# Optimization experiments

Measured on AMD Instinct MI355X. Metric: run time of the kernel, lower is better.

The kernel has to match this reference:

```python
import jax, jax.numpy as jnp
import numpy as np

G, NG, K, D = 64, 2048, 16, 256  # graphs, nodes/graph, eigvecs/graph, feature dim


def setup_inputs() -> dict:
    key = jax.random.key(0)
    k0, k1, k2, k3, k4 = jax.random.split(key, 5)
    x = jax.random.normal(k0, (G * NG, D), jnp.float32)
    # eigenvectors of per-graph Laplacians (values arbitrary for correctness baseline)
    eigvec = jax.random.normal(k1, (G * NG, K), jnp.float32) / np.float32(np.sqrt(NG))
    split_real = jnp.ones((D,), jnp.float32)
    split_imag = jnp.ones((D,), jnp.float32)
    spec_filter = jax.random.uniform(k2, (G, K, D), dtype=jnp.float32)
    W1 = jax.random.normal(k3, (D, D), jnp.float32) / np.float32(np.sqrt(D))
    W2 = jax.random.normal(k4, (D, D), jnp.float32) / np.float32(np.sqrt(D))
    factor_split = jnp.ones((D, 2), jnp.float32)
    return dict(x=x, eigvec=eigvec, split_real=split_real, split_imag=split_imag,
                spec_filter=spec_filter, W1=W1, W2=W2, factor_split=factor_split)


def _silu_norm(h):
    # SiLU gating: sigmoid of complex L2-norm over the spectral (k) axis, keepdim
    norm = jnp.sqrt(jnp.sum(h.real ** 2 + h.imag ** 2, axis=1, keepdims=True))
    return h * jax.nn.sigmoid(norm)


def reference(x, eigvec, split_real, split_imag, spec_filter, W1, W2, factor_split):
    # SpecFeatureTransformLayer (split variant): x -> complex
    xc = jax.lax.complex(split_real * x, split_imag * x)      # [N, D] complex64
    V = eigvec.reshape(G, NG, K)                              # block-diagonal eigvec basis
    xg = xc.reshape(G, NG, D)
    # eigvec^H @ x  (block-diag COO matmul, eigvecs real so conj is a no-op)
    x_spec = jnp.einsum('gnk,gnd->gkd', V, xg)                # [G, K, D] complex64
    x_spec = spec_filter * x_spec                             # learned spectral filter
    # silu_stack: MaybeComplexLinear (same real weight on real & imag) + norm-gated SiLU
    for W in (W1, W2):                                        # W: [out, in], y = x @ W^T
        h = jnp.einsum('gkd,ed->gke', x_spec, W)
        x_spec = _silu_norm(h)
    # project back to node domain: eigvec @ x_spec
    xn = jnp.einsum('gnk,gkd->gnd', V, x_spec).reshape(G * NG, D)
    # real/imag merge via factor_split
    out = xn.real * factor_split[:, 0] + xn.imag * factor_split[:, 1]
    return out + x                                            # node residual
```

## Files before the change

kernel.cpp:

```cpp
#include <hip/hip_runtime.h>
#include <math.h>

#define G  64
#define NG 2048
#define K  16
#define D  256
#define KD (K*D)
#define ROWS 32
#define NCHUNK (NG/ROWS)
#define WPF ((size_t)G * NCHUNK * KD)

typedef float v4f __attribute__((ext_vector_type(4)));

__global__ __launch_bounds__(64) void k_project(const float* __restrict__ x,
                                                const float* __restrict__ eig,
                                                float* __restrict__ WP) {
    __shared__ float sV[ROWS * K];
    const int b  = blockIdx.x;
    const int g  = b >> 6, c = b & 63;
    const int n0 = g * NG + c * ROWS;
    const int t  = threadIdx.x;

    {
        const float4* e4 = (const float4*)(eig + (size_t)n0 * K);
        float4* s4 = (float4*)sV;
        s4[t]      = e4[t];
        s4[t + 64] = e4[t + 64];
    }
    __syncthreads();

    float acc[K][4];
#pragma unroll
    for (int k = 0; k < K; ++k)
#pragma unroll
        for (int j = 0; j < 4; ++j) acc[k][j] = 0.f;

    const float4* x4 = (const float4*)x + (size_t)n0 * 64;
#pragma unroll 4
    for (int n = 0; n < ROWS; ++n) {
        const float4 xv = x4[n * 64 + t];
#pragma unroll
        for (int kq = 0; kq < 4; ++kq) {
            const float4 v = *(const float4*)&sV[n * K + kq * 4];
            acc[kq*4+0][0] += v.x * xv.x; acc[kq*4+0][1] += v.x * xv.y;
            acc[kq*4+0][2] += v.x * xv.z; acc[kq*4+0][3] += v.x * xv.w;
            acc[kq*4+1][0] += v.y * xv.x; acc[kq*4+1][1] += v.y * xv.y;
            acc[kq*4+1][2] += v.y * xv.z; acc[kq*4+1][3] += v.y * xv.w;
            acc[kq*4+2][0] += v.z * xv.x; acc[kq*4+2][1] += v.z * xv.y;
            acc[kq*4+2][2] += v.z * xv.z; acc[kq*4+2][3] += v.z * xv.w;
            acc[kq*4+3][0] += v.w * xv.x; acc[kq*4+3][1] += v.w * xv.y;
            acc[kq*4+3][2] += v.w * xv.z; acc[kq*4+3][3] += v.w * xv.w;
        }
    }

    float4* wp4 = (float4*)WP + (size_t)b * (KD / 4);
#pragma unroll
    for (int k = 0; k < K; ++k)
        wp4[k * 64 + t] = make_float4(acc[k][0], acc[k][1], acc[k][2], acc[k][3]);
}

__global__ __launch_bounds__(256) void k_reduce(const float* __restrict__ WP,
                                                const float* __restrict__ filt,
                                                const float* __restrict__ sr,
                                                const float* __restrict__ si,
                                                float* __restrict__ Xr,
                                                float* __restrict__ Xi) {
    const int b = blockIdx.x;
    const int g = b >> 2, q = b & 3;
    const int f = q * 256 + threadIdx.x;
    const float4* wp4 = (const float4*)WP + (size_t)g * NCHUNK * (KD / 4);
    float ax = 0.f, ay = 0.f, az = 0.f, aw = 0.f;
#pragma unroll 8
    for (int w = 0; w < NCHUNK; ++w) {
        const float4 p = wp4[(size_t)w * (KD / 4) + f];
        ax += p.x; ay += p.y; az += p.z; aw += p.w;
    }
    const float4 fl = ((const float4*)filt)[(size_t)g * (KD / 4) + f];
    const int d4 = f & 63;
    const float4 s0 = ((const float4*)sr)[d4];
    const float4 s1 = ((const float4*)si)[d4];
    float4 xr, xi;
    xr.x = ax * fl.x * s0.x; xr.y = ay * fl.y * s0.y;
    xr.z = az * fl.z * s0.z; xr.w = aw * fl.w * s0.w;
    xi.x = ax * fl.x * s1.x; xi.y = ay * fl.y * s1.y;
    xi.z = az * fl.z * s1.z; xi.w = aw * fl.w * s1.w;
    ((float4*)Xr)[(size_t)g * (KD / 4) + f] = xr;
    ((float4*)Xi)[(size_t)g * (KD / 4) + f] = xi;
}

template <int LAYER>
__global__ __launch_bounds__(256) void k_mlp(const float* __restrict__ Xr,
                                             const float* __restrict__ Xi,
                                             const float* __restrict__ W,
                                             const float* __restrict__ fs,
                                             float* __restrict__ o0,
                                             float* __restrict__ o1) {
    __shared__ float4 sW[64 * 64];
    __shared__ float  sRed[4 * 64 * 8];
    const int b     = blockIdx.x;
    const int g     = b >> 2;
    const int slice = b & 3;
    const int t     = threadIdx.x;

    {
        const float4* Wg = (const float4*)W + (size_t)slice * 64 * 64;
#pragma unroll
        for (int it = 0; it < 16; ++it) {
            const int idx = it * 256 + t;
            const int e = idx >> 6, ds = idx & 63;
            sW[e * 64 + (ds ^ (e & 7))] = Wg[idx];
        }
    }
    __syncthreads();

    const int el = t & 63;
    const int kq = t >> 6;
    const float* xr = Xr + (size_t)g * KD + (kq * 4) * D;
    const float* xi = Xi + (size_t)g * KD + (kq * 4) * D;

    float pr[4] = {0.f, 0.f, 0.f, 0.f};
    float pi[4] = {0.f, 0.f, 0.f, 0.f};
#pragma unroll 4
    for (int ds = 0; ds < 64; ++ds) {
        const float4 w = sW[el * 64 + (ds ^ (el & 7))];
#pragma unroll
        for (int kk = 0; kk < 4; ++kk) {
            const float4 a = *(const float4*)&xr[kk * D + ds * 4];
            const float4 c = *(const float4*)&xi[kk * D + ds * 4];
            pr[kk] += w.x * a.x + w.y * a.y + w.z * a.z + w.w * a.w;
            pi[kk] += w.x * c.x + w.y * c.y + w.z * c.z + w.w * c.w;
        }
    }

#pragma unroll
    for (int kk = 0; kk < 4; ++kk) {
        sRed[(kq * 64 + el) * 8 + kk]     = pr[kk];
        sRed[(kq * 64 + el) * 8 + 4 + kk] = pi[kk];
    }
    __syncthreads();

    if (t < 64) {
        float hr[K], hi[K];
        float nrm = 0.f;
#pragma unroll
        for (int q2 = 0; q2 < 4; ++q2)
#pragma unroll
            for (int kk = 0; kk < 4; ++kk) {
                const float r  = sRed[(q2 * 64 + t) * 8 + kk];
                const float im = sRed[(q2 * 64 + t) * 8 + 4 + kk];
                hr[q2 * 4 + kk] = r; hi[q2 * 4 + kk] = im;
                nrm += r * r + im * im;
            }
        const float sg = 1.f / (1.f + expf(-sqrtf(nrm)));
        const int e = slice * 64 + t;
        if (LAYER == 1) {
#pragma unroll
            for (int k = 0; k < K; ++k) {
                o0[(size_t)g * KD + k * D + e] = hr[k] * sg;
                o1[(size_t)g * KD + k * D + e] = hi[k] * sg;
            }
        } else {
            const float f0 = fs[e * 2], f1 = fs[e * 2 + 1];
#pragma unroll
            for (int k = 0; k < K; ++k)
                o0[(size_t)g * KD + k * D + e] = (hr[k] * sg) * f0 + (hi[k] * sg) * f1;
        }
    }
}

__global__ __launch_bounds__(64) void k_back(const float* __restrict__ x,
                                             const float* __restrict__ eig,
                                             const float* __restrict__ z,
                                             float* __restrict__ out) {
    __shared__ float sV[ROWS * K];
    const int b  = blockIdx.x;
    const int g  = b >> 6, c = b & 63;
    const int n0 = g * NG + c * ROWS;
    const int t  = threadIdx.x;
    {
        const float4* e4 = (const float4*)(eig + (size_t)n0 * K);
        float4* s4 = (float4*)sV;
        s4[t]      = e4[t];
        s4[t + 64] = e4[t + 64];
    }
    float4 zr[K];
    const float4* z4 = (const float4*)z + (size_t)g * (KD / 4);
#pragma unroll
    for (int k = 0; k < K; ++k) zr[k] = z4[k * 64 + t];
    __syncthreads();

    const float4* x4 = (const float4*)x + (size_t)n0 * 64;
    v4f* o4 = (v4f*)out + (size_t)n0 * 64;
#pragma unroll 4
    for (int n = 0; n < ROWS; ++n) {
        float4 o = x4[n * 64 + t];
#pragma unroll
        for (int kq = 0; kq < 4; ++kq) {
            const float4 v = *(const float4*)&sV[n * K + kq * 4];
            o.x += v.x * zr[kq*4+0].x + v.y * zr[kq*4+1].x + v.z * zr[kq*4+2].x + v.w * zr[kq*4+3].x;
            o.y += v.x * zr[kq*4+0].y + v.y * zr[kq*4+1].y + v.z * zr[kq*4+2].y + v.w * zr[kq*4+3].y;
            o.z += v.x * zr[kq*4+0].z + v.y * zr[kq*4+1].z + v.z * zr[kq*4+2].z + v.w * zr[kq*4+3].z;
            o.w += v.x * zr[kq*4+0].w + v.y * zr[kq*4+1].w + v.z * zr[kq*4+2].w + v.w * zr[kq*4+3].w;
        }
        v4f ov; ov.x = o.x; ov.y = o.y; ov.z = o.z; ov.w = o.w;
        __builtin_nontemporal_store(ov, &o4[n * 64 + t]);
    }
}

extern "C" void kernel_launch(void* const* d_in, const int* in_sizes, int n_in,
                              void* d_out, int out_size, void* d_ws, size_t ws_size,
                              hipStream_t stream) {
    const float* x    = (const float*)d_in[0];
    const float* eig  = (const float*)d_in[1];
    const float* sr   = (const float*)d_in[2];
    const float* si   = (const float*)d_in[3];
    const float* filt = (const float*)d_in[4];
    const float* W1   = (const float*)d_in[5];
    const float* W2   = (const float*)d_in[6];
    const float* fs   = (const float*)d_in[7];
    float* out = (float*)d_out;

    float* WP  = out;
    float* Xr  = out + WPF;
    float* Xi  = Xr + (size_t)G * KD;
    float* y1r = Xi + (size_t)G * KD;
    float* y1i = y1r + (size_t)G * KD;
    float* z   = (float*)d_ws;

    k_project<<<G * NCHUNK, 64, 0, stream>>>(x, eig, WP);
    k_reduce<<<G * 4, 256, 0, stream>>>(WP, filt, sr, si, Xr, Xi);
    k_mlp<1><<<G * 4, 256, 0, stream>>>(Xr, Xi, W1, nullptr, y1r, y1i);
    k_mlp<2><<<G * 4, 256, 0, stream>>>(y1r, y1i, W2, fs, z, nullptr);
    k_back<<<G * NCHUNK, 64, 0, stream>>>(x, eig, z, out);
}
```

Measured before the change: 339.0 us.

## Reduce partial sums in-block in projection and widen MLP work split

The projection kernel now uses 256-thread blocks covering 128 rows each, with four wavefronts reducing their partial K×D sums through shared memory. This cuts the number of partial tiles written to global memory and read back by the reduce kernel by a factor of four. The MLP kernels split the output features into 8 slices of 32 with a parallel norm reduction, which doubles the block count and removes the single-wave serial epilogue. The back-projection kernel moves to 256-thread blocks. The cost is extra shared memory (32KB of reduction buffer) and barriers in the projection kernel.

Measured after the change: 316.6 us. 6.6% less time.

```diff
diff --git a/kernel.cpp b/kernel.cpp
--- a/kernel.cpp
+++ b/kernel.cpp
@@ -6,26 +6,29 @@
 #define K  16
 #define D  256
 #define KD (K*D)
-#define ROWS 32
-#define NCHUNK (NG/ROWS)
+#define PROWS 128
+#define NCHUNK (NG/PROWS)
 #define WPF ((size_t)G * NCHUNK * KD)
 
 typedef float v4f __attribute__((ext_vector_type(4)));
 
-__global__ __launch_bounds__(64) void k_project(const float* __restrict__ x,
-                                                const float* __restrict__ eig,
-                                                float* __restrict__ WP) {
-    __shared__ float sV[ROWS * K];
+__global__ __launch_bounds__(256) void k_project(const float* __restrict__ x,
+                                                 const float* __restrict__ eig,
+                                                 float* __restrict__ WP) {
+    __shared__ float sV[PROWS * K];
+    __shared__ float red[2 * KD];
     const int b  = blockIdx.x;
-    const int g  = b >> 6, c = b & 63;
-    const int n0 = g * NG + c * ROWS;
+    const int g  = b >> 4, c = b & 15;
+    const int n0 = g * NG + c * PROWS;
     const int t  = threadIdx.x;
+    const int d4 = t & 63;
+    const int nq = t >> 6;
 
     {
         const float4* e4 = (const float4*)(eig + (size_t)n0 * K);
         float4* s4 = (float4*)sV;
-        s4[t]      = e4[t];
-        s4[t + 64] = e4[t + 64];
+        s4[t]       = e4[t];
+        s4[t + 256] = e4[t + 256];
     }
     __syncthreads();
 
@@ -35,13 +38,14 @@
 #pragma unroll
         for (int j = 0; j < 4; ++j) acc[k][j] = 0.f;
 
-    const float4* x4 = (const float4*)x + (size_t)n0 * 64;
+    const float4* x4 = (const float4*)x + ((size_t)n0 + nq * 32) * 64;
+    const float* vbase = sV + nq * 32 * K;
 #pragma unroll 4
-    for (int n = 0; n < ROWS; ++n) {
-        const float4 xv = x4[n * 64 + t];
+    for (int n = 0; n < 32; ++n) {
+        const float4 xv = x4[n * 64 + d4];
 #pragma unroll
         for (int kq = 0; kq < 4; ++kq) {
-            const float4 v = *(const float4*)&sV[n * K + kq * 4];
+            const float4 v = *(const float4*)&vbase[n * K + kq * 4];
             acc[kq*4+0][0] += v.x * xv.x; acc[kq*4+0][1] += v.x * xv.y;
             acc[kq*4+0][2] += v.x * xv.z; acc[kq*4+0][3] += v.x * xv.w;
             acc[kq*4+1][0] += v.y * xv.x; acc[kq*4+1][1] += v.y * xv.y;
@@ -53,10 +57,37 @@
         }
     }
 
-    float4* wp4 = (float4*)WP + (size_t)b * (KD / 4);
-#pragma unroll
-    for (int k = 0; k < K; ++k)
-        wp4[k * 64 + t] = make_float4(acc[k][0], acc[k][1], acc[k][2], acc[k][3]);
+    if (nq >= 2) {
+#pragma unroll
+        for (int k = 0; k < K; ++k)
+            *(float4*)&red[(nq - 2) * KD + k * D + d4 * 4] =
+                make_float4(acc[k][0], acc[k][1], acc[k][2], acc[k][3]);
+    }
+    __syncthreads();
+    if (nq < 2) {
+#pragma unroll
+        for (int k = 0; k < K; ++k) {
+            const float4 r = *(const float4*)&red[nq * KD + k * D + d4 * 4];
+            acc[k][0] += r.x; acc[k][1] += r.y; acc[k][2] += r.z; acc[k][3] += r.w;
+        }
+    }
+    __syncthreads();
+    if (nq == 1) {
+#pragma unroll
+        for (int k = 0; k < K; ++k)
+            *(float4*)&red[k * D + d4 * 4] =
+                make_float4(acc[k][0], acc[k][1], acc[k][2], acc[k][3]);
+    }
+    __syncthreads();
+    if (nq == 0) {
+        float4* wp4 = (float4*)WP + (size_t)b * (KD / 4);
+#pragma unroll
+        for (int k = 0; k < K; ++k) {
+            const float4 r = *(const float4*)&red[k * D + d4 * 4];
+            wp4[k * 64 + d4] = make_float4(acc[k][0] + r.x, acc[k][1] + r.y,
+                                           acc[k][2] + r.z, acc[k][3] + r.w);
+        }
+    }
 }
 
 __global__ __launch_bounds__(256) void k_reduce(const float* __restrict__ WP,
@@ -70,7 +101,7 @@
     const int f = q * 256 + threadIdx.x;
     const float4* wp4 = (const float4*)WP + (size_t)g * NCHUNK * (KD / 4);
     float ax = 0.f, ay = 0.f, az = 0.f, aw = 0.f;
-#pragma unroll 8
+#pragma unroll
     for (int w = 0; w < NCHUNK; ++w) {
         const float4 p = wp4[(size_t)w * (KD / 4) + f];
         ax += p.x; ay += p.y; az += p.z; aw += p.w;
@@ -89,23 +120,24 @@
 }
 
 template <int LAYER>
-__global__ __launch_bounds__(256) void k_mlp(const float* __restrict__ Xr,
-                                             const float* __restrict__ Xi,
+__global__ __launch_bounds__(256) void k_mlp(const float* __restrict__ Ar,
+                                             const float* __restrict__ Ai,
                                              const float* __restrict__ W,
                                              const float* __restrict__ fs,
                                              float* __restrict__ o0,
                                              float* __restrict__ o1) {
-    __shared__ float4 sW[64 * 64];
-    __shared__ float  sRed[4 * 64 * 8];
+    __shared__ float4 sW[32 * 64];
+    __shared__ float  sNrm[8 * 32];
+    __shared__ float  sSg[32];
     const int b     = blockIdx.x;
-    const int g     = b >> 2;
-    const int slice = b & 3;
+    const int g     = b >> 3;
+    const int slice = b & 7;
     const int t     = threadIdx.x;
 
     {
-        const float4* Wg = (const float4*)W + (size_t)slice * 64 * 64;
-#pragma unroll
-        for (int it = 0; it < 16; ++it) {
+        const float4* Wg = (const float4*)W + (size_t)slice * 32 * 64;
+#pragma unroll
+        for (int it = 0; it < 8; ++it) {
             const int idx = it * 256 + t;
             const int e = idx >> 6, ds = idx & 63;
             sW[e * 64 + (ds ^ (e & 7))] = Wg[idx];
@@ -113,97 +145,88 @@
     }
     __syncthreads();
 
-    const int el = t & 63;
-    const int kq = t >> 6;
-    const float* xr = Xr + (size_t)g * KD + (kq * 4) * D;
-    const float* xi = Xi + (size_t)g * KD + (kq * 4) * D;
-
-    float pr[4] = {0.f, 0.f, 0.f, 0.f};
-    float pi[4] = {0.f, 0.f, 0.f, 0.f};
-#pragma unroll 4
+    const int el = t & 31;
+    const int kg = t >> 5;
+    const int e  = slice * 32 + el;
+    const float* ar = Ar + (size_t)g * KD + (kg * 2) * D;
+    const float* ai = Ai + (size_t)g * KD + (kg * 2) * D;
+
+    float pr0 = 0.f, pr1 = 0.f, pi0 = 0.f, pi1 = 0.f;
+#pragma unroll 8
     for (int ds = 0; ds < 64; ++ds) {
-        const float4 w = sW[el * 64 + (ds ^ (el & 7))];
-#pragma unroll
-        for (int kk = 0; kk < 4; ++kk) {
-            const float4 a = *(const float4*)&xr[kk * D + ds * 4];
-            const float4 c = *(const float4*)&xi[kk * D + ds * 4];
-            pr[kk] += w.x * a.x + w.y * a.y + w.z * a.z + w.w * a.w;
-            pi[kk] += w.x * c.x + w.y * c.y + w.z * c.z + w.w * c.w;
-        }
-    }
-
-#pragma unroll
-    for (int kk = 0; kk < 4; ++kk) {
-        sRed[(kq * 64 + el) * 8 + kk]     = pr[kk];
-        sRed[(kq * 64 + el) * 8 + 4 + kk] = pi[kk];
-    }
-    __syncthreads();
-
-    if (t < 64) {
-        float hr[K], hi[K];
+        const float4 w  = sW[el * 64 + (ds ^ (el & 7))];
+        const float4 a0 = *(const float4*)&ar[ds * 4];
+        const float4 a1 = *(const float4*)&ar[D + ds * 4];
+        const float4 c0 = *(const float4*)&ai[ds * 4];
+        const float4 c1 = *(const float4*)&ai[D + ds * 4];
+        pr0 += w.x * a0.x + w.y * a0.y + w.z * a0.z + w.w * a0.w;
+        pr1 += w.x * a1.x + w.y * a1.y + w.z * a1.z + w.w * a1.w;
+        pi0 += w.x * c0.x + w.y * c0.y + w.z * c0.z + w.w * c0.w;
+        pi1 += w.x * c1.x + w.y * c1.y + w.z * c1.z + w.w * c1.w;
+    }
+
+    sNrm[kg * 32 + el] = pr0 * pr0 + pi0 * pi0 + pr1 * pr1 + pi1 * pi1;
+    __syncthreads();
+    if (t < 32) {
         float nrm = 0.f;
 #pragma unroll
-        for (int q2 = 0; q2 < 4; ++q2)
-#pragma unroll
-            for (int kk = 0; kk < 4; ++kk) {
-                const float r  = sRed[(q2 * 64 + t) * 8 + kk];
-                const float im = sRed[(q2 * 64 + t) * 8 + 4 + kk];
-                hr[q2 * 4 + kk] = r; hi[q2 * 4 + kk] = im;
-                nrm += r * r + im * im;
-            }
-        const float sg = 1.f / (1.f + expf(-sqrtf(nrm)));
-        const int e = slice * 64 + t;
-        if (LAYER == 1) {
-#pragma unroll
-            for (int k = 0; k < K; ++k) {
-                o0[(size_t)g * KD + k * D + e] = hr[k] * sg;
-                o1[(size_t)g * KD + k * D + e] = hi[k] * sg;
-            }
-        } else {
-            const float f0 = fs[e * 2], f1 = fs[e * 2 + 1];
-#pragma unroll
-            for (int k = 0; k < K; ++k)
-                o0[(size_t)g * KD + k * D + e] = (hr[k] * sg) * f0 + (hi[k] * sg) * f1;
-        }
-    }
-}
-
-__global__ __launch_bounds__(64) void k_back(const float* __restrict__ x,
-                                             const float* __restrict__ eig,
-                                             const float* __restrict__ z,
-                                             float* __restrict__ out) {
-    __shared__ float sV[ROWS * K];
+        for (int w = 0; w < 8; ++w) nrm += sNrm[w * 32 + t];
+        sSg[t] = 1.f / (1.f + expf(-sqrtf(nrm)));
+    }
+    __syncthreads();
+    const float sg = sSg[el];
+
+    float* base0 = o0 + (size_t)g * KD + (kg * 2) * D + e;
+    if (LAYER == 1) {
+        float* base1 = o1 + (size_t)g * KD + (kg * 2) * D + e;
+        base0[0] = pr0 * sg; base0[D] = pr1 * sg;
+        base1[0] = pi0 * sg; base1[D] = pi1 * sg;
+    } else {
+        const float f0 = fs[e * 2], f1 = fs[e * 2 + 1];
+        base0[0] = (pr0 * f0 + pi0 * f1) * sg;
+        base0[D] = (pr1 * f0 + pi1 * f1) * sg;
+    }
+}
+
+__global__ __launch_bounds__(256) void k_back(const float* __restrict__ x,
+                                              const float* __restrict__ eig,
+                                              const float* __restrict__ z,
+                                              float* __restrict__ out) {
+    __shared__ float sV[PROWS * K];
     const int b  = blockIdx.x;
-    const int g  = b >> 6, c = b & 63;
-    const int n0 = g * NG + c * ROWS;
+    const int g  = b >> 4, c = b & 15;
+    const int n0 = g * NG + c * PROWS;
     const int t  = threadIdx.x;
+    const int d4 = t & 63;
+    const int nq = t >> 6;
     {
         const float4* e4 = (const float4*)(eig + (size_t)n0 * K);
         float4* s4 = (float4*)sV;
-        s4[t]      = e4[t];
-        s4[t + 64] = e4[t + 64];
+        s4[t]       = e4[t];
+        s4[t + 256] = e4[t + 256];
     }
     float4 zr[K];
     const float4* z4 = (const float4*)z + (size_t)g * (KD / 4);
 #pragma unroll
-    for (int k = 0; k < K; ++k) zr[k] = z4[k * 64 + t];
-    __syncthreads();
-
-    const float4* x4 = (const float4*)x + (size_t)n0 * 64;
-    v4f* o4 = (v4f*)out + (size_t)n0 * 64;
+    for (int k = 0; k < K; ++k) zr[k] = z4[k * 64 + d4];
+    __syncthreads();
+
+    const float4* x4 = (const float4*)x + ((size_t)n0 + nq * 32) * 64;
+    v4f* o4 = (v4f*)out + ((size_t)n0 + nq * 32) * 64;
+    const float* vbase = sV + nq * 32 * K;
 #pragma unroll 4
-    for (int n = 0; n < ROWS; ++n) {
-        float4 o = x4[n * 64 + t];
+    for (int n = 0; n < 32; ++n) {
+        float4 o = x4[n * 64 + d4];
 #pragma unroll
         for (int kq = 0; kq < 4; ++kq) {
-            const float4 v = *(const float4*)&sV[n * K + kq * 4];
+            const float4 v = *(const float4*)&vbase[n * K + kq * 4];
             o.x += v.x * zr[kq*4+0].x + v.y * zr[kq*4+1].x + v.z * zr[kq*4+2].x + v.w * zr[kq*4+3].x;
             o.y += v.x * zr[kq*4+0].y + v.y * zr[kq*4+1].y + v.z * zr[kq*4+2].y + v.w * zr[kq*4+3].y;
             o.z += v.x * zr[kq*4+0].z + v.y * zr[kq*4+1].z + v.z * zr[kq*4+2].z + v.w * zr[kq*4+3].z;
             o.w += v.x * zr[kq*4+0].w + v.y * zr[kq*4+1].w + v.z * zr[kq*4+2].w + v.w * zr[kq*4+3].w;
         }
         v4f ov; ov.x = o.x; ov.y = o.y; ov.z = o.z; ov.w = o.w;
-        __builtin_nontemporal_store(ov, &o4[n * 64 + t]);
+        __builtin_nontemporal_store(ov, &o4[n * 64 + d4]);
     }
 }
 
@@ -227,9 +250,9 @@
     float* y1i = y1r + (size_t)G * KD;
     float* z   = (float*)d_ws;
 
-    k_project<<<G * NCHUNK, 64, 0, stream>>>(x, eig, WP);
+    k_project<<<G * NCHUNK, 256, 0, stream>>>(x, eig, WP);
     k_reduce<<<G * 4, 256, 0, stream>>>(WP, filt, sr, si, Xr, Xi);
-    k_mlp<1><<<G * 4, 256, 0, stream>>>(Xr, Xi, W1, nullptr, y1r, y1i);
-    k_mlp<2><<<G * 4, 256, 0, stream>>>(y1r, y1i, W2, fs, z, nullptr);
-    k_back<<<G * NCHUNK, 64, 0, stream>>>(x, eig, z, out);
-}
+    k_mlp<1><<<G * 8, 256, 0, stream>>>(Xr, Xi, W1, nullptr, y1r, y1i);
+    k_mlp<2><<<G * 8, 256, 0, stream>>>(y1r, y1i, W2, fs, z, nullptr);
+    k_back<<<G * NCHUNK, 256, 0, stream>>>(x, eig, z, out);
+}
```
